# Kernel tuning notes

Hardware: AMD Instinct MI355X
Metric: run time of the kernel (lower is better)

The kernel has to match this reference:

```python
import jax, jax.numpy as jnp
import numpy as np

D = 1024
H = 16
HD = D // H  # 64


def setup_inputs() -> dict:
    key = jax.random.key(0)
    ks = jax.random.split(key, 12)
    B, S = 2, 2048
    inp = {
        "input_query": jax.random.normal(ks[0], (B, S, D), jnp.float32),
        "input_key": jax.random.normal(ks[1], (B, S, D), jnp.float32),
        "input_value": jax.random.normal(ks[2], (B, S, D), jnp.float32),
        "mask": jnp.ones((S, S), dtype=bool),  # ignored, as in original
        # per-head Q/K/V linears, stacked over heads: [H, D, HD]
        "Wq": jax.random.normal(ks[3], (H, D, HD), jnp.float32) / np.sqrt(D),
        "bq": jax.random.normal(ks[4], (H, HD), jnp.float32) * 0.01,
        "Wk": jax.random.normal(ks[5], (H, D, HD), jnp.float32) / np.sqrt(D),
        "bk": jax.random.normal(ks[6], (H, HD), jnp.float32) * 0.01,
        "Wv": jax.random.normal(ks[7], (H, D, HD), jnp.float32) / np.sqrt(D),
        "bv": jax.random.normal(ks[8], (H, HD), jnp.float32) * 0.01,
        "Wo": jax.random.normal(ks[9], (D, D), jnp.float32) / np.sqrt(D),
        "bo": jax.random.normal(ks[10], (D,), jnp.float32) * 0.01,
    }
    return inp


def reference(input_query, input_key, input_value, mask, Wq, bq, Wk, bk, Wv, bv, Wo, bo):
    B, S, _ = input_query.shape
    # batched per-head projections: [B,S,D] x [H,D,HD] -> [B,H,S,HD]
    q = jnp.einsum("bsd,hdk->bhsk", input_query, Wq) + bq[None, :, None, :]
    k = jnp.einsum("bsd,hdk->bhsk", input_key, Wk) + bk[None, :, None, :]
    v = jnp.einsum("bsd,hdk->bhsk", input_value, Wv) + bv[None, :, None, :]
    scale = 1.0 / np.sqrt(HD)
    scores = jnp.einsum("bhqk,bhsk->bhqs", q, k) * scale  # [B,H,S,S]
    causal = jnp.tril(jnp.ones((S, S), dtype=bool))
    scores = jnp.where(causal[None, None], scores, jnp.finfo(scores.dtype).min)
    p = jax.nn.softmax(scores, axis=-1)
    out = jnp.einsum("bhqs,bhsk->bhqk", p, v)  # [B,H,S,HD]
    # concat heads (matches torch.cat over head outputs on last dim)
    out = out.transpose(0, 2, 1, 3).reshape(B, S, D)
    return out @ Wo + bo
```

## Files before the change

kernel.cpp:

```cpp
#include <hip/hip_runtime.h>
#include <hip/hip_bf16.h>

typedef __bf16 bf16;
typedef bf16 bf16x8 __attribute__((ext_vector_type(8)));
typedef bf16 bf16x4 __attribute__((ext_vector_type(4)));
typedef float f32x4 __attribute__((ext_vector_type(4)));

#define B_  2
#define S_  2048
#define D_  1024
#define H_  16
#define HD_ 64
#define M_  4096
#define K_  1024
#define N_  1024

#if __has_builtin(__builtin_amdgcn_exp2f)
#define EXP2F(x) __builtin_amdgcn_exp2f(x)
#else
#define EXP2F(x) exp2f(x)
#endif

__device__ __forceinline__ void gld16(const bf16* g, bf16* l) {
    __builtin_amdgcn_global_load_lds(
        (const __attribute__((address_space(1))) unsigned int*)(g),
        (__attribute__((address_space(3))) unsigned int*)(l), 16, 0, 0);
}
__device__ __forceinline__ void gld16f(const float* g, float* l) {
    __builtin_amdgcn_global_load_lds(
        (const __attribute__((address_space(1))) unsigned int*)(g),
        (__attribute__((address_space(3))) unsigned int*)(l), 16, 0, 0);
}

__global__ void pack_w(const float* __restrict__ wq, const float* __restrict__ wk,
                       const float* __restrict__ wv, const float* __restrict__ wo,
                       bf16* __restrict__ out) {
    int t = blockIdx.y;
    bf16* dst = out + (size_t)t * N_ * K_;
    int o = blockIdx.x * 256 + threadIdx.x;
    int n = o >> 10, k = o & 1023;
    if (t == 3) {
        dst[o] = (bf16)wo[k * D_ + n];
    } else {
        const float* src = (t == 0) ? wq : (t == 1) ? wk : wv;
        dst[o] = (bf16)src[(n >> 6) * (D_ * HD_) + k * HD_ + (n & 63)];
    }
}

__global__ __launch_bounds__(256) void gemm_qkv(
        const float* __restrict__ xq, const float* __restrict__ xk,
        const float* __restrict__ xv, const bf16* __restrict__ Wt,
        const float* __restrict__ bq, const float* __restrict__ bk,
        const float* __restrict__ bv, bf16* __restrict__ QKV) {
    __shared__ __align__(16) float Af[2][128 * 32];
    __shared__ __align__(16) bf16 Bs[2][128 * 32];
    int t = blockIdx.z;
    const float* A = (t == 0) ? xq : (t == 1) ? xk : xv;
    const bf16* W = Wt + (size_t)t * N_ * K_;
    const float* bias = (t == 0) ? bq : (t == 1) ? bk : bv;
    int m0 = blockIdx.x * 128, n0 = blockIdx.y * 128;
    int tid = threadIdx.x;
    int w = tid >> 6, l = tid & 63, lr = l & 15, lg = l >> 4;
    int wr = (w >> 1) * 64, wc = (w & 1) * 64;
    int srow = (l >> 2), scol = (l & 3) * 8;
    size_t aoff[4];
    #pragma unroll
    for (int c = 0; c < 4; c++) {
        int chunk = w * 256 + c * 64 + l;
        int r = chunk >> 3, p = chunk & 7;
        aoff[c] = (size_t)(m0 + r) * K_ + ((p ^ (r & 7)) << 2);
    }
    f32x4 acc[4][4] = {};
    #pragma unroll
    for (int c = 0; c < 4; c++)
        gld16f(A + aoff[c], &Af[0][(w * 256 + c * 64) * 4]);
    #pragma unroll
    for (int c = 0; c < 2; c++) {
        int chunk = w * 2 + c;
        gld16(&W[(size_t)(n0 + chunk * 16 + srow) * K_ + scol], &Bs[0][chunk * 512]);
    }
    __syncthreads();
    for (int k0 = 0; k0 < K_; k0 += 32) {
        int cur = (k0 >> 5) & 1, nxt = cur ^ 1;
        if (k0 + 32 < K_) {
            #pragma unroll
            for (int c = 0; c < 4; c++)
                gld16f(A + aoff[c] + k0 + 32, &Af[nxt][(w * 256 + c * 64) * 4]);
            #pragma unroll
            for (int c = 0; c < 2; c++) {
                int chunk = w * 2 + c;
                gld16(&W[(size_t)(n0 + chunk * 16 + srow) * K_ + k0 + 32 + scol], &Bs[nxt][chunk * 512]);
            }
        }
        bf16x8 af[4], bfr[4];
        #pragma unroll
        for (int mi = 0; mi < 4; mi++) {
            int r = wr + mi * 16 + lr;
            f32x4 a0 = *(const f32x4*)((const char*)Af[cur] + r * 128 + (((lg * 2) ^ (r & 7)) * 16));
            f32x4 a1 = *(const f32x4*)((const char*)Af[cur] + r * 128 + (((lg * 2 + 1) ^ (r & 7)) * 16));
            bf16x8 v = { (bf16)a0[0], (bf16)a0[1], (bf16)a0[2], (bf16)a0[3],
                         (bf16)a1[0], (bf16)a1[1], (bf16)a1[2], (bf16)a1[3] };
            af[mi] = v;
        }
        #pragma unroll
        for (int ni = 0; ni < 4; ni++) bfr[ni] = *(const bf16x8*)&Bs[cur][(wc + ni * 16 + lr) * 32 + lg * 8];
        #pragma unroll
        for (int mi = 0; mi < 4; mi++)
            #pragma unroll
            for (int ni = 0; ni < 4; ni++)
                acc[mi][ni] = __builtin_amdgcn_mfma_f32_16x16x32_bf16(af[mi], bfr[ni], acc[mi][ni], 0, 0, 0);
        __syncthreads();
    }
    float qscale = (t == 0) ? 0.125f * 1.4426950408889634f : 1.0f;
    #pragma unroll
    for (int mi = 0; mi < 4; mi++)
        #pragma unroll
        for (int ni = 0; ni < 4; ni++)
            #pragma unroll
            for (int i = 0; i < 4; i++) {
                int m = m0 + wr + mi * 16 + lg * 4 + i;
                int n = n0 + wc + ni * 16 + lr;
                float v = (acc[mi][ni][i] + bias[n]) * qscale;
                int b = m >> 11, s = m & 2047, h = n >> 6, hd = n & 63;
                QKV[((((size_t)t * B_ + b) * H_ + h) * S_ + s) * HD_ + hd] = (bf16)v;
            }
}

__global__ __launch_bounds__(256) void gemm_out(
        const bf16* __restrict__ A, const bf16* __restrict__ Wt,
        const float* __restrict__ bo, float* __restrict__ out) {
    __shared__ __align__(16) bf16 As[2][128 * 32];
    __shared__ __align__(16) bf16 Bs[2][128 * 32];
    int m0 = blockIdx.x * 128, n0 = blockIdx.y * 128;
    int tid = threadIdx.x;
    int w = tid >> 6, l = tid & 63, lr = l & 15, lg = l >> 4;
    int wr = (w >> 1) * 64, wc = (w & 1) * 64;
    int srow = (l >> 2), scol = (l & 3) * 8;
    f32x4 acc[4][4] = {};
    #pragma unroll
    for (int c = 0; c < 2; c++) {
        int chunk = w * 2 + c;
        gld16(&A[(size_t)(m0 + chunk * 16 + srow) * K_ + scol], &As[0][chunk * 512]);
        gld16(&Wt[(size_t)(n0 + chunk * 16 + srow) * K_ + scol], &Bs[0][chunk * 512]);
    }
    __syncthreads();
    for (int k0 = 0; k0 < K_; k0 += 32) {
        int cur = (k0 >> 5) & 1, nxt = cur ^ 1;
        if (k0 + 32 < K_) {
            #pragma unroll
            for (int c = 0; c < 2; c++) {
                int chunk = w * 2 + c;
                gld16(&A[(size_t)(m0 + chunk * 16 + srow) * K_ + k0 + 32 + scol], &As[nxt][chunk * 512]);
                gld16(&Wt[(size_t)(n0 + chunk * 16 + srow) * K_ + k0 + 32 + scol], &Bs[nxt][chunk * 512]);
            }
        }
        bf16x8 af[4], bfr[4];
        #pragma unroll
        for (int mi = 0; mi < 4; mi++) af[mi] = *(const bf16x8*)&As[cur][(wr + mi * 16 + lr) * 32 + lg * 8];
        #pragma unroll
        for (int ni = 0; ni < 4; ni++) bfr[ni] = *(const bf16x8*)&Bs[cur][(wc + ni * 16 + lr) * 32 + lg * 8];
        #pragma unroll
        for (int mi = 0; mi < 4; mi++)
            #pragma unroll
            for (int ni = 0; ni < 4; ni++)
                acc[mi][ni] = __builtin_amdgcn_mfma_f32_16x16x32_bf16(af[mi], bfr[ni], acc[mi][ni], 0, 0, 0);
        __syncthreads();
    }
    #pragma unroll
    for (int mi = 0; mi < 4; mi++)
        #pragma unroll
        for (int ni = 0; ni < 4; ni++)
            #pragma unroll
            for (int i = 0; i < 4; i++) {
                int m = m0 + wr + mi * 16 + lg * 4 + i;
                int n = n0 + wc + ni * 16 + lr;
                out[(size_t)m * N_ + n] = acc[mi][ni][i] + bo[n];
            }
}

__global__ __launch_bounds__(256) void transpose_v(const bf16* __restrict__ V,
                                                   bf16* __restrict__ VT) {
    __shared__ __align__(16) bf16 Ls[64][64];
    int s0 = blockIdx.x * 64, bh = blockIdx.y;
    const bf16* src = V + (size_t)bh * S_ * HD_;
    bf16* dst = VT + (size_t)bh * HD_ * S_;
    int tid = threadIdx.x;
    #pragma unroll
    for (int c = tid; c < 512; c += 256) {
        int row = c >> 3, cg = (c & 7) * 8;
        int cgp = cg ^ (((row >> 3) & 3) << 4);
        *(bf16x8*)&Ls[row][cgp] = *(const bf16x8*)&src[(size_t)(s0 + row) * 64 + cg];
    }
    __syncthreads();
    #pragma unroll
    for (int c = tid; c < 512; c += 256) {
        int hd = c >> 3, sg = (c & 7) * 8;
        bf16x8 v;
        #pragma unroll
        for (int e = 0; e < 8; e++) {
            int row = sg + e;
            v[e] = Ls[row][hd ^ (((row >> 3) & 3) << 4)];
        }
        *(bf16x8*)&dst[(size_t)hd * S_ + s0 + sg] = v;
    }
}

__global__ __launch_bounds__(512) void attn(const bf16* __restrict__ QKV,
                                            const bf16* __restrict__ VT,
                                            bf16* __restrict__ AO) {
    __shared__ __align__(16) bf16 Ks[2][64][72];
    __shared__ __align__(16) bf16 Vts[2][64][72];
    __shared__ __align__(16) bf16 Ps2[8][16][16][4];
    int bh = blockIdx.y;
    int qt = (bh & 16) ? blockIdx.x : (15 - blockIdx.x);
    int q0 = qt * 128;
    const bf16* Qp = QKV + (size_t)bh * S_ * HD_;
    const bf16* Kp = QKV + (size_t)(32 + bh) * S_ * HD_;
    const bf16* VTp = VT + (size_t)bh * HD_ * S_;
    int tid = threadIdx.x, w = tid >> 6, l = tid & 63, lr = l & 15, lg = l >> 4;
    int srow = tid >> 3, scg = (tid & 7) * 8;

    bf16x8 aq[2];
    #pragma unroll
    for (int ks = 0; ks < 2; ks++)
        aq[ks] = *(const bf16x8*)&Qp[(size_t)(q0 + w * 16 + lr) * 64 + ks * 32 + lg * 8];

    f32x4 o[4] = {};
    float lsum = 0.0f;
    int jmax = 2 * qt + 1;

    *(bf16x8*)&Ks[0][srow][scg]  = *(const bf16x8*)&Kp[(size_t)srow * 64 + scg];
    *(bf16x8*)&Vts[0][srow][scg] = *(const bf16x8*)&VTp[(size_t)srow * S_ + scg];
    __syncthreads();

    for (int j = 0; j <= jmax; ++j) {
        int cur = j & 1;
        bool pf = (j < jmax);
        bf16x8 kreg, vreg;
        if (pf) {
            kreg = *(const bf16x8*)&Kp[(size_t)((j + 1) * 64 + srow) * 64 + scg];
            vreg = *(const bf16x8*)&VTp[(size_t)srow * S_ + (j + 1) * 64 + scg];
        }

        f32x4 sc[4] = {};
        __builtin_amdgcn_s_setprio(1);
        #pragma unroll
        for (int ks = 0; ks < 2; ks++)
            #pragma unroll
            for (int ni = 0; ni < 4; ni++) {
                bf16x8 bk_ = *(const bf16x8*)&Ks[cur][ni * 16 + lr][ks * 32 + lg * 8];
                sc[ni] = __builtin_amdgcn_mfma_f32_16x16x32_bf16(bk_, aq[ks], sc[ni], 0, 0, 0);
            }
        __builtin_amdgcn_s_setprio(0);

        int kvb = j * 64 - q0;
        if (j >= 2 * qt) {
            #pragma unroll
            for (int ni = 0; ni < 4; ni++) {
                float pv[4];
                #pragma unroll
                for (int i = 0; i < 4; i++) {
                    float s = sc[ni][i];
                    if (kvb + ni * 16 + lg * 4 + i > w * 16 + lr) s = -30000.0f;
                    float p = EXP2F(s);
                    lsum += p;
                    pv[i] = p;
                }
                bf16x4 pk = { (bf16)pv[0], (bf16)pv[1], (bf16)pv[2], (bf16)pv[3] };
                *(bf16x4*)&Ps2[w][ni * 4 + lg][lr][0] = pk;
            }
        } else {
            #pragma unroll
            for (int ni = 0; ni < 4; ni++) {
                float pv[4];
                #pragma unroll
                for (int i = 0; i < 4; i++) {
                    float p = EXP2F(sc[ni][i]);
                    lsum += p;
                    pv[i] = p;
                }
                bf16x4 pk = { (bf16)pv[0], (bf16)pv[1], (bf16)pv[2], (bf16)pv[3] };
                *(bf16x4*)&Ps2[w][ni * 4 + lg][lr][0] = pk;
            }
        }

        __builtin_amdgcn_s_setprio(1);
        #pragma unroll
        for (int ks = 0; ks < 2; ks++) {
            bf16x4 lo = *(const bf16x4*)&Ps2[w][8 * ks + 2 * lg + 0][lr][0];
            bf16x4 hi = *(const bf16x4*)&Ps2[w][8 * ks + 2 * lg + 1][lr][0];
            bf16x8 bq = __builtin_shufflevector(lo, hi, 0, 1, 2, 3, 4, 5, 6, 7);
            #pragma unroll
            for (int nf = 0; nf < 4; nf++) {
                bf16x8 bv_ = *(const bf16x8*)&Vts[cur][nf * 16 + lr][ks * 32 + lg * 8];
                o[nf] = __builtin_amdgcn_mfma_f32_16x16x32_bf16(bv_, bq, o[nf], 0, 0, 0);
            }
        }
        __builtin_amdgcn_s_setprio(0);

        if (pf) {
            *(bf16x8*)&Ks[cur ^ 1][srow][scg]  = kreg;
            *(bf16x8*)&Vts[cur ^ 1][srow][scg] = vreg;
        }
        __syncthreads();
    }

    lsum += __shfl_xor(lsum, 16);
    lsum += __shfl_xor(lsum, 32);
    float inv = 1.0f / lsum;

    int b = bh >> 4, h = bh & 15;
    int m = b * S_ + q0 + w * 16 + lr;
    #pragma unroll
    for (int nf = 0; nf < 4; nf++) {
        bf16x4 ov = { (bf16)(o[nf][0] * inv), (bf16)(o[nf][1] * inv),
                      (bf16)(o[nf][2] * inv), (bf16)(o[nf][3] * inv) };
        *(bf16x4*)&AO[(size_t)m * D_ + h * 64 + nf * 16 + lg * 4] = ov;
    }
}

extern "C" void kernel_launch(void* const* d_in, const int* in_sizes, int n_in,
                              void* d_out, int out_size, void* d_ws, size_t ws_size,
                              hipStream_t stream) {
    const float* xq = (const float*)d_in[0];
    const float* xk = (const float*)d_in[1];
    const float* xv = (const float*)d_in[2];
    const float* wq = (const float*)d_in[4];
    const float* bq = (const float*)d_in[5];
    const float* wk = (const float*)d_in[6];
    const float* bk = (const float*)d_in[7];
    const float* wv = (const float*)d_in[8];
    const float* bv = (const float*)d_in[9];
    const float* wo = (const float*)d_in[10];
    const float* bo = (const float*)d_in[11];
    float* out = (float*)d_out;

    bf16* Xb  = (bf16*)d_ws;
    bf16* Wb  = Xb  + (size_t)3 * M_ * K_;
    bf16* WoT = Wb  + (size_t)3 * N_ * K_;
    bf16* QKV = WoT + (size_t)N_ * K_;
    bf16* AO  = QKV + (size_t)3 * M_ * K_;
    bf16* VT  = Xb;

    pack_w <<<dim3(N_ * K_ / 256, 4), 256, 0, stream>>>(wq, wk, wv, wo, Wb);
    gemm_qkv<<<dim3(M_ / 128, N_ / 128, 3), 256, 0, stream>>>(xq, xk, xv, Wb, bq, bk, bv, QKV);
    transpose_v<<<dim3(S_ / 64, B_ * H_), 256, 0, stream>>>(QKV + (size_t)2 * M_ * K_, VT);
    attn    <<<dim3(S_ / 128, B_ * H_), 512, 0, stream>>>(QKV, VT, AO);
    gemm_out<<<dim3(M_ / 128, N_ / 128), 256, 0, stream>>>(AO, WoT, bo, out);
}
```

Baseline: 127.0 us.

## Triple-buffer GEMM LDS stages with single barrier and partial vmcnt waits

Both projection GEMMs move from a double-buffered K loop with two-stage prefetch to a three-buffer ring. Each iteration does one explicit s_waitcnt with a nonzero vmcnt and one s_barrier, so one stage's global-to-LDS loads can still be in flight while the current tile is computed. This is meant to hide global load latency and remove the trailing __syncthreads per step. In exchange it uses more LDS, which may lower occupancy, especially for the fp32 A buffers in gemm_qkv, and it depends on hand-set vmcnt values being correct.

```diff
diff --git a/kernel.cpp b/kernel.cpp
--- a/kernel.cpp
+++ b/kernel.cpp
@@ -52,8 +52,8 @@
         const float* __restrict__ xv, const bf16* __restrict__ Wt,
         const float* __restrict__ bq, const float* __restrict__ bk,
         const float* __restrict__ bv, bf16* __restrict__ QKV) {
-    __shared__ __align__(16) float Af[2][128 * 32];
-    __shared__ __align__(16) bf16 Bs[2][128 * 32];
+    __shared__ __align__(16) float Af[3][128 * 32];
+    __shared__ __align__(16) bf16 Bs[3][128 * 32];
     int t = blockIdx.z;
     const float* A = (t == 0) ? xq : (t == 1) ? xk : xv;
     const bf16* W = Wt + (size_t)t * N_ * K_;
@@ -71,46 +71,48 @@
         aoff[c] = (size_t)(m0 + r) * K_ + ((p ^ (r & 7)) << 2);
     }
     f32x4 acc[4][4] = {};
-    #pragma unroll
-    for (int c = 0; c < 4; c++)
-        gld16f(A + aoff[c], &Af[0][(w * 256 + c * 64) * 4]);
-    #pragma unroll
-    for (int c = 0; c < 2; c++) {
-        int chunk = w * 2 + c;
-        gld16(&W[(size_t)(n0 + chunk * 16 + srow) * K_ + scol], &Bs[0][chunk * 512]);
-    }
-    __syncthreads();
-    for (int k0 = 0; k0 < K_; k0 += 32) {
-        int cur = (k0 >> 5) & 1, nxt = cur ^ 1;
-        if (k0 + 32 < K_) {
-            #pragma unroll
-            for (int c = 0; c < 4; c++)
-                gld16f(A + aoff[c] + k0 + 32, &Af[nxt][(w * 256 + c * 64) * 4]);
-            #pragma unroll
-            for (int c = 0; c < 2; c++) {
-                int chunk = w * 2 + c;
-                gld16(&W[(size_t)(n0 + chunk * 16 + srow) * K_ + k0 + 32 + scol], &Bs[nxt][chunk * 512]);
-            }
-        }
+
+    auto stage = [&](int buf, int k0) {
+        #pragma unroll
+        for (int c = 0; c < 4; c++)
+            gld16f(A + aoff[c] + k0, &Af[buf][(w * 256 + c * 64) * 4]);
+        #pragma unroll
+        for (int c = 0; c < 2; c++) {
+            int chunk = w * 2 + c;
+            gld16(&W[(size_t)(n0 + chunk * 16 + srow) * K_ + k0 + scol], &Bs[buf][chunk * 512]);
+        }
+    };
+    auto do_step = [&](int cb) {
         bf16x8 af[4], bfr[4];
         #pragma unroll
         for (int mi = 0; mi < 4; mi++) {
             int r = wr + mi * 16 + lr;
-            f32x4 a0 = *(const f32x4*)((const char*)Af[cur] + r * 128 + (((lg * 2) ^ (r & 7)) * 16));
-            f32x4 a1 = *(const f32x4*)((const char*)Af[cur] + r * 128 + (((lg * 2 + 1) ^ (r & 7)) * 16));
+            f32x4 a0 = *(const f32x4*)((const char*)Af[cb] + r * 128 + (((lg * 2) ^ (r & 7)) * 16));
+            f32x4 a1 = *(const f32x4*)((const char*)Af[cb] + r * 128 + (((lg * 2 + 1) ^ (r & 7)) * 16));
             bf16x8 v = { (bf16)a0[0], (bf16)a0[1], (bf16)a0[2], (bf16)a0[3],
                          (bf16)a1[0], (bf16)a1[1], (bf16)a1[2], (bf16)a1[3] };
             af[mi] = v;
         }
         #pragma unroll
-        for (int ni = 0; ni < 4; ni++) bfr[ni] = *(const bf16x8*)&Bs[cur][(wc + ni * 16 + lr) * 32 + lg * 8];
+        for (int ni = 0; ni < 4; ni++) bfr[ni] = *(const bf16x8*)&Bs[cb][(wc + ni * 16 + lr) * 32 + lg * 8];
         #pragma unroll
         for (int mi = 0; mi < 4; mi++)
             #pragma unroll
             for (int ni = 0; ni < 4; ni++)
                 acc[mi][ni] = __builtin_amdgcn_mfma_f32_16x16x32_bf16(af[mi], bfr[ni], acc[mi][ni], 0, 0, 0);
-        __syncthreads();
-    }
+    };
+
+    stage(0, 0);
+    stage(1, 32);
+    #pragma unroll 3
+    for (int i = 0; i < 31; i++) {
+        asm volatile("s_waitcnt vmcnt(6) lgkmcnt(0)\n\ts_barrier" ::: "memory");
+        if (i < 30) stage((i + 2) % 3, (i + 2) * 32);
+        do_step(i % 3);
+    }
+    asm volatile("s_waitcnt vmcnt(0) lgkmcnt(0)\n\ts_barrier" ::: "memory");
+    do_step(31 % 3);
+
     float qscale = (t == 0) ? 0.125f * 1.4426950408889634f : 1.0f;
     #pragma unroll
     for (int mi = 0; mi < 4; mi++)
@@ -129,43 +131,47 @@
 __global__ __launch_bounds__(256) void gemm_out(
         const bf16* __restrict__ A, const bf16* __restrict__ Wt,
         const float* __restrict__ bo, float* __restrict__ out) {
-    __shared__ __align__(16) bf16 As[2][128 * 32];
-    __shared__ __align__(16) bf16 Bs[2][128 * 32];
+    __shared__ __align__(16) bf16 As[3][128 * 32];
+    __shared__ __align__(16) bf16 Bs[3][128 * 32];
     int m0 = blockIdx.x * 128, n0 = blockIdx.y * 128;
     int tid = threadIdx.x;
     int w = tid >> 6, l = tid & 63, lr = l & 15, lg = l >> 4;
     int wr = (w >> 1) * 64, wc = (w & 1) * 64;
     int srow = (l >> 2), scol = (l & 3) * 8;
     f32x4 acc[4][4] = {};
-    #pragma unroll
-    for (int c = 0; c < 2; c++) {
-        int chunk = w * 2 + c;
-        gld16(&A[(size_t)(m0 + chunk * 16 + srow) * K_ + scol], &As[0][chunk * 512]);
-        gld16(&Wt[(size_t)(n0 + chunk * 16 + srow) * K_ + scol], &Bs[0][chunk * 512]);
-    }
-    __syncthreads();
-    for (int k0 = 0; k0 < K_; k0 += 32) {
-        int cur = (k0 >> 5) & 1, nxt = cur ^ 1;
-        if (k0 + 32 < K_) {
-            #pragma unroll
-            for (int c = 0; c < 2; c++) {
-                int chunk = w * 2 + c;
-                gld16(&A[(size_t)(m0 + chunk * 16 + srow) * K_ + k0 + 32 + scol], &As[nxt][chunk * 512]);
-                gld16(&Wt[(size_t)(n0 + chunk * 16 + srow) * K_ + k0 + 32 + scol], &Bs[nxt][chunk * 512]);
-            }
-        }
+
+    auto stage = [&](int buf, int k0) {
+        #pragma unroll
+        for (int c = 0; c < 2; c++) {
+            int chunk = w * 2 + c;
+            gld16(&A[(size_t)(m0 + chunk * 16 + srow) * K_ + k0 + scol], &As[buf][chunk * 512]);
+            gld16(&Wt[(size_t)(n0 + chunk * 16 + srow) * K_ + k0 + scol], &Bs[buf][chunk * 512]);
+        }
+    };
+    auto do_step = [&](int cb) {
         bf16x8 af[4], bfr[4];
         #pragma unroll
-        for (int mi = 0; mi < 4; mi++) af[mi] = *(const bf16x8*)&As[cur][(wr + mi * 16 + lr) * 32 + lg * 8];
-        #pragma unroll
-        for (int ni = 0; ni < 4; ni++) bfr[ni] = *(const bf16x8*)&Bs[cur][(wc + ni * 16 + lr) * 32 + lg * 8];
+        for (int mi = 0; mi < 4; mi++) af[mi] = *(const bf16x8*)&As[cb][(wr + mi * 16 + lr) * 32 + lg * 8];
+        #pragma unroll
+        for (int ni = 0; ni < 4; ni++) bfr[ni] = *(const bf16x8*)&Bs[cb][(wc + ni * 16 + lr) * 32 + lg * 8];
         #pragma unroll
         for (int mi = 0; mi < 4; mi++)
             #pragma unroll
             for (int ni = 0; ni < 4; ni++)
                 acc[mi][ni] = __builtin_amdgcn_mfma_f32_16x16x32_bf16(af[mi], bfr[ni], acc[mi][ni], 0, 0, 0);
-        __syncthreads();
-    }
+    };
+
+    stage(0, 0);
+    stage(1, 32);
+    #pragma unroll 3
+    for (int i = 0; i < 31; i++) {
+        asm volatile("s_waitcnt vmcnt(4) lgkmcnt(0)\n\ts_barrier" ::: "memory");
+        if (i < 30) stage((i + 2) % 3, (i + 2) * 32);
+        do_step(i % 3);
+    }
+    asm volatile("s_waitcnt vmcnt(0) lgkmcnt(0)\n\ts_barrier" ::: "memory");
+    do_step(31 % 3);
+
     #pragma unroll
     for (int mi = 0; mi < 4; mi++)
         #pragma unroll
```

After: 147.7 us. 16.4% more time.

## Pre-convert activations to bf16 and widen QKV GEMM tiles to 128x256

Applied to the files above, without the earlier changes.

Adds a pack_x kernel that converts the fp32 query/key/value inputs to bf16 in the workspace before the projection GEMM. The GEMM then streams bf16 A tiles directly into LDS instead of loading fp32 tiles and converting them inside the inner loop. The block tile grows to 128x256 with 512 threads, which halves the number of blocks and increases reuse of each A tile. The cost is an extra full pass over the inputs (read fp32, write bf16), and the LDS layout drops the previous XOR swizzle, so bank conflicts may appear.

```diff
diff --git a/kernel.cpp b/kernel.cpp
--- a/kernel.cpp
+++ b/kernel.cpp
@@ -26,10 +26,16 @@
         (const __attribute__((address_space(1))) unsigned int*)(g),
         (__attribute__((address_space(3))) unsigned int*)(l), 16, 0, 0);
 }
-__device__ __forceinline__ void gld16f(const float* g, float* l) {
-    __builtin_amdgcn_global_load_lds(
-        (const __attribute__((address_space(1))) unsigned int*)(g),
-        (__attribute__((address_space(3))) unsigned int*)(l), 16, 0, 0);
+
+__global__ void pack_x(const float* __restrict__ xq, const float* __restrict__ xk,
+                       const float* __restrict__ xv, bf16* __restrict__ out) {
+    int t = blockIdx.y;
+    const float* src = (t == 0) ? xq : (t == 1) ? xk : xv;
+    bf16* dst = out + (size_t)t * M_ * K_;
+    int idx = (blockIdx.x * 256 + threadIdx.x) * 4;
+    float4 v = *(const float4*)&src[idx];
+    bf16x4 o = { (bf16)v.x, (bf16)v.y, (bf16)v.z, (bf16)v.w };
+    *(bf16x4*)&dst[idx] = o;
 }
 
 __global__ void pack_w(const float* __restrict__ wq, const float* __restrict__ wk,
@@ -47,70 +53,60 @@
     }
 }
 
-__global__ __launch_bounds__(256) void gemm_qkv(
-        const float* __restrict__ xq, const float* __restrict__ xk,
-        const float* __restrict__ xv, const bf16* __restrict__ Wt,
+__global__ __launch_bounds__(512) void gemm_qkv(
+        const bf16* __restrict__ X, const bf16* __restrict__ Wt,
         const float* __restrict__ bq, const float* __restrict__ bk,
         const float* __restrict__ bv, bf16* __restrict__ QKV) {
-    __shared__ __align__(16) float Af[2][128 * 32];
-    __shared__ __align__(16) bf16 Bs[2][128 * 32];
+    __shared__ __align__(16) bf16 As[2][128 * 32];
+    __shared__ __align__(16) bf16 Bs[2][256 * 32];
     int t = blockIdx.z;
-    const float* A = (t == 0) ? xq : (t == 1) ? xk : xv;
+    const bf16* A = X + (size_t)t * M_ * K_;
     const bf16* W = Wt + (size_t)t * N_ * K_;
     const float* bias = (t == 0) ? bq : (t == 1) ? bk : bv;
-    int m0 = blockIdx.x * 128, n0 = blockIdx.y * 128;
+    int m0 = blockIdx.x * 128, n0 = blockIdx.y * 256;
     int tid = threadIdx.x;
     int w = tid >> 6, l = tid & 63, lr = l & 15, lg = l >> 4;
-    int wr = (w >> 1) * 64, wc = (w & 1) * 64;
-    int srow = (l >> 2), scol = (l & 3) * 8;
-    size_t aoff[4];
-    #pragma unroll
-    for (int c = 0; c < 4; c++) {
-        int chunk = w * 256 + c * 64 + l;
-        int r = chunk >> 3, p = chunk & 7;
-        aoff[c] = (size_t)(m0 + r) * K_ + ((p ^ (r & 7)) << 2);
+    int wr = (w >> 2) * 64, wc = (w & 3) * 64;
+    int ac = w * 64 + l;
+    size_t aoffg = (size_t)(m0 + (ac >> 2)) * K_ + (ac & 3) * 8;
+    size_t boffg[2];
+    #pragma unroll
+    for (int c = 0; c < 2; c++) {
+        int chunk = w * 128 + c * 64 + l;
+        boffg[c] = (size_t)(n0 + (chunk >> 2)) * K_ + (chunk & 3) * 8;
     }
     f32x4 acc[4][4] = {};
-    #pragma unroll
-    for (int c = 0; c < 4; c++)
-        gld16f(A + aoff[c], &Af[0][(w * 256 + c * 64) * 4]);
-    #pragma unroll
-    for (int c = 0; c < 2; c++) {
-        int chunk = w * 2 + c;
-        gld16(&W[(size_t)(n0 + chunk * 16 + srow) * K_ + scol], &Bs[0][chunk * 512]);
-    }
+
+    auto stage = [&](int buf, int k0) {
+        gld16(&A[aoffg + k0], &As[buf][ac * 8]);
+        #pragma unroll
+        for (int c = 0; c < 2; c++)
+            gld16(&W[boffg[c] + k0], &Bs[buf][(w * 128 + c * 64) * 8]);
+    };
+    auto do_step = [&](int cb) {
+        bf16x8 af[4], bfr[4];
+        #pragma unroll
+        for (int mi = 0; mi < 4; mi++)
+            af[mi] = *(const bf16x8*)&As[cb][(wr + mi * 16 + lr) * 32 + lg * 8];
+        #pragma unroll
+        for (int ni = 0; ni < 4; ni++)
+            bfr[ni] = *(const bf16x8*)&Bs[cb][(wc + ni * 16 + lr) * 32 + lg * 8];
+        #pragma unroll
+        for (int mi = 0; mi < 4; mi++)
+            #pragma unroll
+            for (int ni = 0; ni < 4; ni++)
+                acc[mi][ni] = __builtin_amdgcn_mfma_f32_16x16x32_bf16(af[mi], bfr[ni], acc[mi][ni], 0, 0, 0);
+    };
+
+    stage(0, 0);
     __syncthreads();
     for (int k0 = 0; k0 < K_; k0 += 32) {
         int cur = (k0 >> 5) & 1, nxt = cur ^ 1;
-        if (k0 + 32 < K_) {
-            #pragma unroll
-            for (int c = 0; c < 4; c++)
-                gld16f(A + aoff[c] + k0 + 32, &Af[nxt][(w * 256 + c * 64) * 4]);
-            #pragma unroll
-            for (int c = 0; c < 2; c++) {
-                int chunk = w * 2 + c;
-                gld16(&W[(size_t)(n0 + chunk * 16 + srow) * K_ + k0 + 32 + scol], &Bs[nxt][chunk * 512]);
-            }
-        }
-        bf16x8 af[4], bfr[4];
-        #pragma unroll
-        for (int mi = 0; mi < 4; mi++) {
-            int r = wr + mi * 16 + lr;
-            f32x4 a0 = *(const f32x4*)((const char*)Af[cur] + r * 128 + (((lg * 2) ^ (r & 7)) * 16));
-            f32x4 a1 = *(const f32x4*)((const char*)Af[cur] + r * 128 + (((lg * 2 + 1) ^ (r & 7)) * 16));
-            bf16x8 v = { (bf16)a0[0], (bf16)a0[1], (bf16)a0[2], (bf16)a0[3],
-                         (bf16)a1[0], (bf16)a1[1], (bf16)a1[2], (bf16)a1[3] };
-            af[mi] = v;
-        }
-        #pragma unroll
-        for (int ni = 0; ni < 4; ni++) bfr[ni] = *(const bf16x8*)&Bs[cur][(wc + ni * 16 + lr) * 32 + lg * 8];
-        #pragma unroll
-        for (int mi = 0; mi < 4; mi++)
-            #pragma unroll
-            for (int ni = 0; ni < 4; ni++)
-                acc[mi][ni] = __builtin_amdgcn_mfma_f32_16x16x32_bf16(af[mi], bfr[ni], acc[mi][ni], 0, 0, 0);
+        if (k0 + 32 < K_) stage(nxt, k0 + 32);
+        do_step(cur);
         __syncthreads();
     }
+
     float qscale = (t == 0) ? 0.125f * 1.4426950408889634f : 1.0f;
     #pragma unroll
     for (int mi = 0; mi < 4; mi++)
@@ -342,8 +338,9 @@
     bf16* AO  = QKV + (size_t)3 * M_ * K_;
     bf16* VT  = Xb;
 
+    pack_x <<<dim3(M_ * K_ / 1024, 3), 256, 0, stream>>>(xq, xk, xv, Xb);
     pack_w <<<dim3(N_ * K_ / 256, 4), 256, 0, stream>>>(wq, wk, wv, wo, Wb);
-    gemm_qkv<<<dim3(M_ / 128, N_ / 128, 3), 256, 0, stream>>>(xq, xk, xv, Wb, bq, bk, bv, QKV);
+    gemm_qkv<<<dim3(M_ / 128, N_ / 256, 3), 512, 0, stream>>>(Xb, Wb, bq, bk, bv, QKV);
     transpose_v<<<dim3(S_ / 64, B_ * H_), 256, 0, stream>>>(QKV + (size_t)2 * M_ * K_, VT);
     attn    <<<dim3(S_ / 128, B_ * H_), 512, 0, stream>>>(QKV, VT, AO);
     gemm_out<<<dim3(M_ / 128, N_ / 128), 256, 0, stream>>>(AO, WoT, bo, out);
```

After: 132.6 us. +4.4%, slower.
